# Performance work log

Hardware: AMD Instinct MI355X
Metric: run time of the kernel (lower is better)

## Reference

```python
import jax, jax.numpy as jnp
import numpy as np

B, S, D, H = 2, 2048, 1024, 16
D_H = D // H  # 64


def setup_inputs() -> dict:
    key = jax.random.key(0)
    ks = jax.random.split(key, 12)
    inp = {
        "query": jax.random.normal(ks[0], (B, S, D), dtype=jnp.float32),
        "key":   jax.random.normal(ks[1], (B, S, D), dtype=jnp.float32),
        "value": jax.random.normal(ks[2], (B, S, D), dtype=jnp.float32),
        # causal 0/1 float mask, broadcastable to [B, H, Sq, Sk]; 1 = masked
        "mask":  jnp.broadcast_to(jnp.triu(jnp.ones((S, S), dtype=jnp.float32), k=1)[None, None], (B, 1, S, S)),
    }
    scale = 0.02
    inp["wq"] = jax.random.normal(ks[3], (D, D), dtype=jnp.float32) * scale
    inp["bq"] = jnp.zeros((D,), dtype=jnp.float32)
    inp["wk"] = jax.random.normal(ks[4], (D, D), dtype=jnp.float32) * scale
    inp["bk"] = jnp.zeros((D,), dtype=jnp.float32)
    inp["wv"] = jax.random.normal(ks[5], (D, D), dtype=jnp.float32) * scale
    inp["bv"] = jnp.zeros((D,), dtype=jnp.float32)
    inp["wff"] = jax.random.normal(ks[6], (D, D), dtype=jnp.float32) * scale
    inp["bff"] = jnp.zeros((D,), dtype=jnp.float32)
    return inp


def _split_head(x):
    # [B, S, D] -> [B, H, S, d_h]
    b, s, _ = x.shape
    return x.reshape(b, s, H, D_H).transpose(0, 2, 1, 3)


def reference(query, key, value, mask, wq, bq, wk, bk, wv, bv, wff, bff):
    # QKV projections (torch Linear: x @ W.T + b)
    q = _split_head(query @ wq.T + bq)
    k = _split_head(key @ wk.T + bk)
    v = _split_head(value @ wv.T + bv)
    # scaled dot-product attention
    scores = jnp.einsum("bhqd,bhkd->bhqk", q, k) / jnp.sqrt(jnp.float32(D_H))
    scores = scores + mask * (-1e9)
    attn = jax.nn.softmax(scores, axis=-1)
    out = jnp.einsum("bhqk,bhkd->bhqd", attn, v)
    # concat heads: [B, H, S, d_h] -> [B, S, D]
    out = out.transpose(0, 2, 1, 3).reshape(query.shape[0], query.shape[1], D)
    return out @ wff.T + bff
```

## Files before the change

kernel.cpp:

```cpp
#include <hip/hip_runtime.h>
#include <hip/hip_bf16.h>

#define B_  2
#define S_  2048
#define D_  1024
#define H_  16
#define DH_ 64
#define M_  (B_ * S_)

using bf16x8 = __attribute__((ext_vector_type(8))) short;
using s16x4  = __attribute__((ext_vector_type(4))) short;
using f32x4  = __attribute__((ext_vector_type(4))) float;

__device__ __forceinline__ bf16x8 ldg8(const __hip_bfloat16* p) {
    bf16x8 v;
    __builtin_memcpy(&v, p, 16);
    return v;
}
__device__ __forceinline__ bf16x8 lds8(const __hip_bfloat16* p) {
    bf16x8 v;
    __builtin_memcpy(&v, p, 16);
    return v;
}
__device__ __forceinline__ void gll16(const void* g, void* l) {
    __builtin_amdgcn_global_load_lds(
        (const __attribute__((address_space(1))) unsigned int*)g,
        (__attribute__((address_space(3))) unsigned int*)l,
        16, 0, 0);
}
__device__ __forceinline__ short bf16bits(float x) {
    __hip_bfloat16 hv = __float2bfloat16(x);
    short sv;
    __builtin_memcpy(&sv, &hv, 2);
    return sv;
}
__device__ __forceinline__ unsigned cvtpk(float lo, float hi) {
    unsigned r;
    asm("v_cvt_pk_bf16_f32 %0, %1, %2" : "=v"(r) : "v"(lo), "v"(hi));
    return r;
}

__global__ void cvt_all(const float* __restrict__ q, const float* __restrict__ k,
                        const float* __restrict__ v, const float* __restrict__ wq,
                        const float* __restrict__ wk, const float* __restrict__ wv,
                        const float* __restrict__ wff,
                        __hip_bfloat16* __restrict__ Xq, __hip_bfloat16* __restrict__ Xk,
                        __hip_bfloat16* __restrict__ Xv, __hip_bfloat16* __restrict__ Wq,
                        __hip_bfloat16* __restrict__ Wk, __hip_bfloat16* __restrict__ Wv,
                        __hip_bfloat16* __restrict__ Wf) {
    const size_t e = (size_t)(blockIdx.x * 256 + threadIdx.x) * 8;
    const float* src;
    __hip_bfloat16* dst;
    size_t off;
    if (e < ((size_t)3 << 22)) {
        const int i = (int)(e >> 22);
        off = e & (((size_t)1 << 22) - 1);
        src = (i == 0) ? q : (i == 1) ? k : v;
        dst = (i == 0) ? Xq : (i == 1) ? Xk : Xv;
    } else {
        const size_t e2 = e - ((size_t)3 << 22);
        const int i = (int)(e2 >> 20);
        off = e2 & (((size_t)1 << 20) - 1);
        src = (i == 0) ? wq : (i == 1) ? wk : (i == 2) ? wv : wff;
        dst = (i == 0) ? Wq : (i == 1) ? Wk : (i == 2) ? Wv : Wf;
    }
    float4 a, b;
    __builtin_memcpy(&a, src + off, 16);
    __builtin_memcpy(&b, src + off + 4, 16);
    __hip_bfloat16 h[8];
    h[0] = __float2bfloat16(a.x); h[1] = __float2bfloat16(a.y);
    h[2] = __float2bfloat16(a.z); h[3] = __float2bfloat16(a.w);
    h[4] = __float2bfloat16(b.x); h[5] = __float2bfloat16(b.y);
    h[6] = __float2bfloat16(b.z); h[7] = __float2bfloat16(b.w);
    __builtin_memcpy(dst + off, h, 16);
}

template<int MI>
__device__ __forceinline__
void gemm_body(const __hip_bfloat16* __restrict__ A,
               const __hip_bfloat16* __restrict__ W,
               const float* __restrict__ bias,
               void* __restrict__ out, int mode, float oscale) {
    constexpr int K  = D_;
    constexpr int N  = D_;
    constexpr int TM = MI * 32;
    __shared__ __hip_bfloat16 At[2][TM][32];
    __shared__ __hip_bfloat16 Wt[2][128][32];

    const int tid = threadIdx.x;
    const int w   = tid >> 6;
    const int l   = tid & 63;
    const int lr  = l & 15;
    const int lg  = l >> 4;
    const int wr  = (w >> 1) * (MI * 16);
    const int wc  = (w & 1) * 64;
    const int row0 = blockIdx.y * TM;
    const int col0 = blockIdx.x * 128;

    const int srow   = l >> 2;
    const int schunk = l & 3;

    f32x4 acc[MI][4] = {};

    auto STAGE = [&](int buf, int k0) {
#pragma unroll
        for (int r = 0; r < TM / 64; ++r) {
            const int row = r * 64 + w * 16 + srow;
            const int csw = (schunk ^ (row & 3)) * 8;
            gll16(A + (size_t)(row0 + row) * K + k0 + csw, &At[buf][r * 64 + w * 16][0]);
        }
#pragma unroll
        for (int r = 0; r < 2; ++r) {
            const int row = r * 64 + w * 16 + srow;
            const int csw = (schunk ^ (row & 3)) * 8;
            gll16(W + (size_t)(col0 + row) * K + k0 + csw, &Wt[buf][r * 64 + w * 16][0]);
        }
    };

    STAGE(0, 0);
    int cur = 0;
    for (int k0 = 0; k0 < K; k0 += 32) {
        __syncthreads();
        if (k0 + 32 < K) STAGE(cur ^ 1, k0 + 32);
        bf16x8 af[MI], wf[4];
#pragma unroll
        for (int m = 0; m < MI; ++m) {
            const int arow = wr + m * 16 + lr;
            af[m] = lds8(&At[cur][arow][(lg ^ (arow & 3)) * 8]);
        }
#pragma unroll
        for (int n = 0; n < 4; ++n) {
            const int wrow = wc + n * 16 + lr;
            wf[n] = lds8(&Wt[cur][wrow][(lg ^ (wrow & 3)) * 8]);
        }
#pragma unroll
        for (int m = 0; m < MI; ++m)
#pragma unroll
            for (int n = 0; n < 4; ++n)
                acc[m][n] = __builtin_amdgcn_mfma_f32_16x16x32_bf16(
                    af[m], wf[n], acc[m][n], 0, 0, 0);
        cur ^= 1;
    }

    float bv[4];
#pragma unroll
    for (int n = 0; n < 4; ++n) bv[n] = bias[col0 + wc + n * 16 + lr];

    if (mode == 1) {
#pragma unroll
        for (int m = 0; m < MI; ++m) {
            const int row_s = row0 + wr + m * 16 + lg * 4;
            const int bq = row_s >> 11, s0 = row_s & (S_ - 1);
#pragma unroll
            for (int n = 0; n < 4; ++n) {
                const int col = col0 + wc + n * 16 + lr;
                const int h = col >> 6, d = col & (DH_ - 1);
                s16x4 pk;
#pragma unroll
                for (int r = 0; r < 4; ++r) pk[r] = bf16bits(acc[m][n][r] + bv[n]);
                __builtin_memcpy(
                    (__hip_bfloat16*)out + ((size_t)((bq * H_ + h) * DH_) + d) * S_ + s0,
                    &pk, 8);
            }
        }
    } else {
#pragma unroll
        for (int m = 0; m < MI; ++m)
#pragma unroll
            for (int n = 0; n < 4; ++n)
#pragma unroll
                for (int r = 0; r < 4; ++r) {
                    const int row = row0 + wr + m * 16 + lg * 4 + r;
                    const int col = col0 + wc + n * 16 + lr;
                    const float v = acc[m][n][r] + bv[n];
                    if (mode == 0)
                        ((__hip_bfloat16*)out)[(size_t)row * N + col] =
                            __float2bfloat16(v * oscale);
                    else
                        ((float*)out)[(size_t)row * N + col] = v;
                }
    }
}

__global__ __launch_bounds__(256)
void gemm_qkv(const __hip_bfloat16* __restrict__ Xq, const __hip_bfloat16* __restrict__ Xk,
              const __hip_bfloat16* __restrict__ Xv, const __hip_bfloat16* __restrict__ Wq,
              const __hip_bfloat16* __restrict__ Wk, const __hip_bfloat16* __restrict__ Wv,
              const float* __restrict__ bq, const float* __restrict__ bk,
              const float* __restrict__ bv,
              __hip_bfloat16* __restrict__ Qp, __hip_bfloat16* __restrict__ Kp,
              __hip_bfloat16* __restrict__ Vt) {
    const int z = blockIdx.z;
    const __hip_bfloat16* A = (z == 0) ? Xq : (z == 1) ? Xk : Xv;
    const __hip_bfloat16* W = (z == 0) ? Wq : (z == 1) ? Wk : Wv;
    const float* bias       = (z == 0) ? bq : (z == 1) ? bk : bv;
    void* out               = (z == 0) ? (void*)Qp : (z == 1) ? (void*)Kp : (void*)Vt;
    const float osc = (z == 0) ? 0.125f * 1.4426950408889634f : 1.f;
    gemm_body<4>(A, W, bias, out, (z == 2) ? 1 : 0, osc);
}

__global__ __launch_bounds__(256)
void gemm_ff(const __hip_bfloat16* __restrict__ A, const __hip_bfloat16* __restrict__ W,
             const float* __restrict__ bias, float* __restrict__ out) {
    gemm_body<2>(A, W, bias, out, 2, 1.f);
}

__global__ __launch_bounds__(512)
void attn_fwd(const __hip_bfloat16* __restrict__ Qp,
              const __hip_bfloat16* __restrict__ Kp,
              const __hip_bfloat16* __restrict__ Vt,
              __hip_bfloat16* __restrict__ O) {
    __shared__ __hip_bfloat16 Kt[2][64][64];
    __shared__ __hip_bfloat16 Vs[2][64][64];
    __shared__ __hip_bfloat16 Pl[8][16][64];

    const int tid = threadIdx.x;
    const int w   = tid >> 6;
    const int l   = tid & 63;
    const int lr  = l & 15;
    const int lg  = l >> 4;

    const int raw = blockIdx.x;
    const int wg  = (raw & 7) * 64 + (raw >> 3);
    const int xcd = wg >> 6;
    const int loc = wg & 63;
    const int bhi = loc >> 4;
    const int prr = loc & 15;
    const int pr  = (bhi >= 2) ? (15 - prr) : prr;
    const int bh  = xcd * 4 + bhi;
    const int h   = bh & (H_ - 1);
    const int b   = bh >> 4;

    const int sub  = w >> 2;
    const int qb_s = sub ? (31 - pr) : pr;
    const int qw0  = qb_s * 64 + (w & 3) * 16;

    bf16x8 aq[2];
#pragma unroll
    for (int kc = 0; kc < 2; ++kc)
        aq[kc] = ldg8(Qp + (size_t)(b * S_ + qw0 + lr) * D_ + h * DH_ + kc * 32 + lg * 8);

    f32x4 o[4] = {};
    f32x4 rs4 = {};

    const int nkt_max = 32 - pr;

    const int srow   = l >> 3;
    const int schunk = l & 7;
    const int psw    = (lr & 7) << 4;

    auto STAGE = [&](int buf, int kt) {
        const int k0 = kt * 64;
        const int row = w * 8 + srow;
        const int csw = (schunk ^ (row & 7)) * 8;
        gll16(Kp + (size_t)(b * S_ + k0 + row) * D_ + h * DH_ + csw,
              &Kt[buf][w * 8][0]);
        gll16(Vt + ((size_t)((b * H_ + h) * DH_) + row) * S_ + k0 + csw,
              &Vs[buf][w * 8][0]);
    };

    char* prow = (char*)&Pl[w][lr][0];

    auto STEP = [&](int kt, int cur) {
        const int k0 = kt * 64;
        __syncthreads();
        if (kt + 1 < nkt_max) STAGE(cur ^ 1, kt + 1);

        if (kt <= qb_s) {
            f32x4 sc[4] = {};
            __builtin_amdgcn_s_setprio(1);
#pragma unroll
            for (int kk = 0; kk < 4; ++kk) {
                const int krow = kk * 16 + lr;
#pragma unroll
                for (int kc = 0; kc < 2; ++kc) {
                    bf16x8 kf = lds8(&Kt[cur][krow][((kc * 4 + lg) ^ (krow & 7)) * 8]);
                    sc[kk] = __builtin_amdgcn_mfma_f32_16x16x32_bf16(kf, aq[kc], sc[kk], 0, 0, 0);
                }
            }
            __builtin_amdgcn_s_setprio(0);

            const int qrow = qw0 + lr;
            if (kt == qb_s) {
#pragma unroll
                for (int kk = 0; kk < 4; ++kk) {
                    float pv[4];
#pragma unroll
                    for (int r = 0; r < 4; ++r) {
                        const int key = k0 + kk * 16 + lg * 4 + r;
                        pv[r] = (key > qrow) ? 0.f : exp2f(sc[kk][r]);
                        rs4[r] += pv[r];
                    }
                    unsigned uu[2] = { cvtpk(pv[0], pv[1]), cvtpk(pv[2], pv[3]) };
                    __builtin_memcpy(prow + ((kk * 32 + lg * 8) ^ psw), uu, 8);
                }
            } else {
#pragma unroll
                for (int kk = 0; kk < 4; ++kk) {
                    float pv[4];
#pragma unroll
                    for (int r = 0; r < 4; ++r) {
                        pv[r] = exp2f(sc[kk][r]);
                        rs4[r] += pv[r];
                    }
                    unsigned uu[2] = { cvtpk(pv[0], pv[1]), cvtpk(pv[2], pv[3]) };
                    __builtin_memcpy(prow + ((kk * 32 + lg * 8) ^ psw), uu, 8);
                }
            }

            bf16x8 pa[2];
#pragma unroll
            for (int kc = 0; kc < 2; ++kc)
                __builtin_memcpy(&pa[kc], prow + ((kc * 64 + lg * 16) ^ psw), 16);
            __builtin_amdgcn_s_setprio(1);
#pragma unroll
            for (int j = 0; j < 4; ++j) {
                const int vrow = j * 16 + lr;
#pragma unroll
                for (int kc = 0; kc < 2; ++kc) {
                    bf16x8 vf = lds8(&Vs[cur][vrow][((kc * 4 + lg) ^ (vrow & 7)) * 8]);
                    o[j] = __builtin_amdgcn_mfma_f32_16x16x32_bf16(pa[kc], vf, o[j], 0, 0, 0);
                }
            }
            __builtin_amdgcn_s_setprio(0);
        }
    };

    STAGE(0, 0);
    for (int kt = 0; kt < nkt_max; kt += 2) {
        STEP(kt, 0);
        if (kt + 1 < nkt_max) STEP(kt + 1, 1);
    }

    float rsf = rs4[0] + rs4[1] + rs4[2] + rs4[3];
    rsf += __shfl_xor(rsf, 16);
    rsf += __shfl_xor(rsf, 32);
#pragma unroll
    for (int r = 0; r < 4; ++r) {
        const float inv = 1.f / __shfl(rsf, 4 * lg + r);
        const int row = qw0 + 4 * lg + r;
#pragma unroll
        for (int j = 0; j < 4; ++j)
            O[((size_t)(b * S_ + row)) * D_ + h * DH_ + j * 16 + lr] =
                __float2bfloat16(o[j][r] * inv);
    }
}

extern "C" void kernel_launch(void* const* d_in, const int* in_sizes, int n_in,
                              void* d_out, int out_size, void* d_ws, size_t ws_size,
                              hipStream_t stream) {
    const float* q    = (const float*)d_in[0];
    const float* kin  = (const float*)d_in[1];
    const float* vin  = (const float*)d_in[2];
    const float* wq   = (const float*)d_in[4];
    const float* bq   = (const float*)d_in[5];
    const float* wk   = (const float*)d_in[6];
    const float* bk   = (const float*)d_in[7];
    const float* wv   = (const float*)d_in[8];
    const float* bv   = (const float*)d_in[9];
    const float* wff  = (const float*)d_in[10];
    const float* bff  = (const float*)d_in[11];

    char* ws = (char*)d_ws;
    const size_t MB = 1024 * 1024;
    __hip_bfloat16* Xq  = (__hip_bfloat16*)(ws + 0 * MB);
    __hip_bfloat16* Xk  = (__hip_bfloat16*)(ws + 8 * MB);
    __hip_bfloat16* Xv  = (__hip_bfloat16*)(ws + 16 * MB);
    __hip_bfloat16* Wqb = (__hip_bfloat16*)(ws + 24 * MB);
    __hip_bfloat16* Wkb = (__hip_bfloat16*)(ws + 26 * MB);
    __hip_bfloat16* Wvb = (__hip_bfloat16*)(ws + 28 * MB);
    __hip_bfloat16* Wfb = (__hip_bfloat16*)(ws + 30 * MB);
    __hip_bfloat16* Qp  = (__hip_bfloat16*)(ws + 32 * MB);
    __hip_bfloat16* Kp  = (__hip_bfloat16*)(ws + 40 * MB);
    __hip_bfloat16* Vt  = (__hip_bfloat16*)(ws + 48 * MB);
    __hip_bfloat16* Ob  = (__hip_bfloat16*)(ws + 56 * MB);

    cvt_all<<<8192, 256, 0, stream>>>(q, kin, vin, wq, wk, wv, wff,
                                      Xq, Xk, Xv, Wqb, Wkb, Wvb, Wfb);

    dim3 gq(D_ / 128, M_ / 128, 3);
    gemm_qkv<<<gq, 256, 0, stream>>>(Xq, Xk, Xv, Wqb, Wkb, Wvb,
                                     bq, bk, bv, Qp, Kp, Vt);

    attn_fwd<<<512, 512, 0, stream>>>(Qp, Kp, Vt, Ob);

    dim3 gg(D_ / 128, M_ / 64);
    gemm_ff<<<gg, 256, 0, stream>>>(Ob, Wfb, bff, (float*)d_out);
}
```

Measured before the change: 123.0 us.

## Remap GEMM tiles per XCD and serialize attention query-block pairs in 256-thread blocks

The GEMM kernels now map linear block IDs so that each XCD works on a contiguous group of row tiles, which should improve L2 reuse of A rows. The attention kernel goes from 512 threads covering two query blocks at once to 256 threads that process the paired blocks (pr and 31-pr) one after the other. K/V staging is reused across the two subtiles, and the next subtile's first tile is prefetched. This balances the causal work and cuts per-block LDS and registers, but the K/V loads for the two halves are no longer shared, and each block runs a longer serial loop.

```diff
diff --git a/kernel.cpp b/kernel.cpp
--- a/kernel.cpp
+++ b/kernel.cpp
@@ -80,7 +80,8 @@
 void gemm_body(const __hip_bfloat16* __restrict__ A,
                const __hip_bfloat16* __restrict__ W,
                const float* __restrict__ bias,
-               void* __restrict__ out, int mode, float oscale) {
+               void* __restrict__ out, int mode, float oscale,
+               int row0, int col0) {
     constexpr int K  = D_;
     constexpr int N  = D_;
     constexpr int TM = MI * 32;
@@ -94,8 +95,6 @@
     const int lg  = l >> 4;
     const int wr  = (w >> 1) * (MI * 16);
     const int wc  = (w & 1) * 64;
-    const int row0 = blockIdx.y * TM;
-    const int col0 = blockIdx.x * 128;
 
     const int srow   = l >> 2;
     const int schunk = l & 3;
@@ -196,23 +195,35 @@
     const float* bias       = (z == 0) ? bq : (z == 1) ? bk : bv;
     void* out               = (z == 0) ? (void*)Qp : (z == 1) ? (void*)Kp : (void*)Vt;
     const float osc = (z == 0) ? 0.125f * 1.4426950408889634f : 1.f;
-    gemm_body<4>(A, W, bias, out, (z == 2) ? 1 : 0, osc);
+
+    const int lin  = blockIdx.y * 8 + blockIdx.x;
+    const int xcd  = lin & 7;
+    const int idx  = lin >> 3;
+    const int row0 = (xcd * 4 + (idx & 3)) * 128;
+    const int col0 = (idx >> 2) * 128;
+
+    gemm_body<4>(A, W, bias, out, (z == 2) ? 1 : 0, osc, row0, col0);
 }
 
 __global__ __launch_bounds__(256)
 void gemm_ff(const __hip_bfloat16* __restrict__ A, const __hip_bfloat16* __restrict__ W,
              const float* __restrict__ bias, float* __restrict__ out) {
-    gemm_body<2>(A, W, bias, out, 2, 1.f);
-}
-
-__global__ __launch_bounds__(512)
+    const int lin  = blockIdx.y * 8 + blockIdx.x;
+    const int xcd  = lin & 7;
+    const int idx  = lin >> 3;
+    const int row0 = (xcd * 8 + (idx & 7)) * 64;
+    const int col0 = (idx >> 3) * 128;
+    gemm_body<2>(A, W, bias, out, 2, 1.f, row0, col0);
+}
+
+__global__ __launch_bounds__(256)
 void attn_fwd(const __hip_bfloat16* __restrict__ Qp,
               const __hip_bfloat16* __restrict__ Kp,
               const __hip_bfloat16* __restrict__ Vt,
               __hip_bfloat16* __restrict__ O) {
     __shared__ __hip_bfloat16 Kt[2][64][64];
     __shared__ __hip_bfloat16 Vs[2][64][64];
-    __shared__ __hip_bfloat16 Pl[8][16][64];
+    __shared__ __hip_bfloat16 Pl[4][16][64];
 
     const int tid = threadIdx.x;
     const int w   = tid >> 6;
@@ -222,28 +233,10 @@
 
     const int raw = blockIdx.x;
     const int wg  = (raw & 7) * 64 + (raw >> 3);
-    const int xcd = wg >> 6;
-    const int loc = wg & 63;
-    const int bhi = loc >> 4;
-    const int prr = loc & 15;
-    const int pr  = (bhi >= 2) ? (15 - prr) : prr;
-    const int bh  = xcd * 4 + bhi;
+    const int bh  = wg >> 4;
+    const int pr  = wg & 15;
     const int h   = bh & (H_ - 1);
     const int b   = bh >> 4;
-
-    const int sub  = w >> 2;
-    const int qb_s = sub ? (31 - pr) : pr;
-    const int qw0  = qb_s * 64 + (w & 3) * 16;
-
-    bf16x8 aq[2];
-#pragma unroll
-    for (int kc = 0; kc < 2; ++kc)
-        aq[kc] = ldg8(Qp + (size_t)(b * S_ + qw0 + lr) * D_ + h * DH_ + kc * 32 + lg * 8);
-
-    f32x4 o[4] = {};
-    f32x4 rs4 = {};
-
-    const int nkt_max = 32 - pr;
 
     const int srow   = l >> 3;
     const int schunk = l & 7;
@@ -251,22 +244,42 @@
 
     auto STAGE = [&](int buf, int kt) {
         const int k0 = kt * 64;
-        const int row = w * 8 + srow;
-        const int csw = (schunk ^ (row & 7)) * 8;
-        gll16(Kp + (size_t)(b * S_ + k0 + row) * D_ + h * DH_ + csw,
-              &Kt[buf][w * 8][0]);
-        gll16(Vt + ((size_t)((b * H_ + h) * DH_) + row) * S_ + k0 + csw,
-              &Vs[buf][w * 8][0]);
+#pragma unroll
+        for (int r = 0; r < 2; ++r) {
+            const int row = w * 16 + r * 8 + srow;
+            const int csw = (schunk ^ (row & 7)) * 8;
+            gll16(Kp + (size_t)(b * S_ + k0 + row) * D_ + h * DH_ + csw,
+                  &Kt[buf][w * 16 + r * 8][0]);
+            gll16(Vt + ((size_t)((b * H_ + h) * DH_) + row) * S_ + k0 + csw,
+                  &Vs[buf][w * 16 + r * 8][0]);
+        }
     };
 
+    const int qb0 = pr, qb1 = 31 - pr;
+    bf16x8 aq0[2], aq1[2];
+#pragma unroll
+    for (int kc = 0; kc < 2; ++kc) {
+        aq0[kc] = ldg8(Qp + (size_t)(b * S_ + qb0 * 64 + w * 16 + lr) * D_ +
+                       h * DH_ + kc * 32 + lg * 8);
+        aq1[kc] = ldg8(Qp + (size_t)(b * S_ + qb1 * 64 + w * 16 + lr) * D_ +
+                       h * DH_ + kc * 32 + lg * 8);
+    }
+
     char* prow = (char*)&Pl[w][lr][0];
-
-    auto STEP = [&](int kt, int cur) {
-        const int k0 = kt * 64;
-        __syncthreads();
-        if (kt + 1 < nkt_max) STAGE(cur ^ 1, kt + 1);
-
-        if (kt <= qb_s) {
+    int cur = 0;
+
+    auto SUBTILE = [&](int qb, bf16x8 (&aq)[2], bool first) {
+        const int qw0  = qb * 64 + w * 16;
+        const int qrow = qw0 + lr;
+        f32x4 o[4] = {};
+        f32x4 rs4 = {};
+
+        for (int kt = 0; kt <= qb; ++kt) {
+            const int k0 = kt * 64;
+            __syncthreads();
+            if (kt < qb) STAGE(cur ^ 1, kt + 1);
+            else if (first) STAGE(cur ^ 1, 0);
+
             f32x4 sc[4] = {};
             __builtin_amdgcn_s_setprio(1);
 #pragma unroll
@@ -280,8 +293,7 @@
             }
             __builtin_amdgcn_s_setprio(0);
 
-            const int qrow = qw0 + lr;
-            if (kt == qb_s) {
+            if (kt == qb) {
 #pragma unroll
                 for (int kk = 0; kk < 4; ++kk) {
                     float pv[4];
@@ -323,27 +335,26 @@
                 }
             }
             __builtin_amdgcn_s_setprio(0);
+            cur ^= 1;
+        }
+
+        float rsf = rs4[0] + rs4[1] + rs4[2] + rs4[3];
+        rsf += __shfl_xor(rsf, 16);
+        rsf += __shfl_xor(rsf, 32);
+#pragma unroll
+        for (int r = 0; r < 4; ++r) {
+            const float inv = 1.f / __shfl(rsf, 4 * lg + r);
+            const int row = qw0 + 4 * lg + r;
+#pragma unroll
+            for (int j = 0; j < 4; ++j)
+                O[((size_t)(b * S_ + row)) * D_ + h * DH_ + j * 16 + lr] =
+                    __float2bfloat16(o[j][r] * inv);
         }
     };
 
     STAGE(0, 0);
-    for (int kt = 0; kt < nkt_max; kt += 2) {
-        STEP(kt, 0);
-        if (kt + 1 < nkt_max) STEP(kt + 1, 1);
-    }
-
-    float rsf = rs4[0] + rs4[1] + rs4[2] + rs4[3];
-    rsf += __shfl_xor(rsf, 16);
-    rsf += __shfl_xor(rsf, 32);
-#pragma unroll
-    for (int r = 0; r < 4; ++r) {
-        const float inv = 1.f / __shfl(rsf, 4 * lg + r);
-        const int row = qw0 + 4 * lg + r;
-#pragma unroll
-        for (int j = 0; j < 4; ++j)
-            O[((size_t)(b * S_ + row)) * D_ + h * DH_ + j * 16 + lr] =
-                __float2bfloat16(o[j][r] * inv);
-    }
+    SUBTILE(qb0, aq0, true);
+    SUBTILE(qb1, aq1, false);
 }
 
 extern "C" void kernel_launch(void* const* d_in, const int* in_sizes, int n_in,
@@ -378,12 +389,12 @@
     cvt_all<<<8192, 256, 0, stream>>>(q, kin, vin, wq, wk, wv, wff,
                                       Xq, Xk, Xv, Wqb, Wkb, Wvb, Wfb);
 
-    dim3 gq(D_ / 128, M_ / 128, 3);
+    dim3 gq(8, 32, 3);
     gemm_qkv<<<gq, 256, 0, stream>>>(Xq, Xk, Xv, Wqb, Wkb, Wvb,
                                      bq, bk, bv, Qp, Kp, Vt);
 
-    attn_fwd<<<512, 512, 0, stream>>>(Qp, Kp, Vt, Ob);
-
-    dim3 gg(D_ / 128, M_ / 64);
+    attn_fwd<<<512, 256, 0, stream>>>(Qp, Kp, Vt, Ob);
+
+    dim3 gg(8, 64);
     gemm_ff<<<gg, 256, 0, stream>>>(Ob, Wfb, bff, (float*)d_out);
 }
```

After: 121.7 us. No clear change (-1.0%).
